# Performance work log

Hardware: AMD Instinct MI355X
Metric: run time of the kernel (lower is better)

The kernel has to match this reference:

```python
import jax, jax.numpy as jnp
import numpy as np

B, H, K, NUM_PTR, MAX_LEN = 32768, 896, 2000, 2, 128


def setup_inputs() -> dict:
    key = jax.random.key(0)
    k1, k2, k3 = jax.random.split(key, 3)
    z = jax.random.normal(k1, (B, H), dtype=jnp.float32)
    # codebook init: normal(0, 0.02) as in torch.nn.init.normal_
    emb = 0.02 * jax.random.normal(k2, (K, H), dtype=jnp.float32)
    # pointer heads: two Linear(H, MAX_LEN) layers, stacked
    W = jax.random.normal(k3, (NUM_PTR, MAX_LEN, H), dtype=jnp.float32) / np.float32(np.sqrt(H))
    b = jnp.zeros((NUM_PTR, MAX_LEN), dtype=jnp.float32)
    return {"z": z, "emb": emb, "W": W, "b": b, "prompt_len": 96}


def reference(z, emb, W, b, prompt_len):
    # --- quantize: L2 cdist + argmin + gather + straight-through ---
    # dist[b,k] = ||z_b||^2 - 2 z_b . e_k + ||e_k||^2   -> [B, K]
    dist = (jnp.sum(z * z, axis=1, keepdims=True)
            - 2.0 * (z @ emb.T)
            + jnp.sum(emb * emb, axis=1)[None, :])
    idx = jnp.argmin(dist, axis=1)            # [B]
    z_q = emb[idx]                            # [B, H]
    op_state = z + jax.lax.stop_gradient(z_q - z)
    # --- pointer heads with prompt-length mask ---
    logits = jnp.einsum('bh,plh->bpl', z, W) + b[None, :, :]   # [B, 2, MAX_LEN]
    mask = jnp.where(jnp.arange(logits.shape[-1]) < prompt_len, 0.0, -jnp.inf)
    ptr_logits = logits + mask[None, None, :]
    return op_state, ptr_logits
```

## Files before the change

### kernel.cpp

```cpp
#include <hip/hip_runtime.h>
#include <hip/hip_bf16.h>
#include <cstdint>
#include <cstddef>

#define B_SZ 32768
#define H_SZ 896
#define K_SZ 2000
#define KPAD 2048
#define NPTR_COLS 256
#define NCAT 2304
#define BM 128
#define BN 128
#define BK 32

typedef float floatx4 __attribute__((ext_vector_type(4)));
typedef __bf16 bf16x8 __attribute__((ext_vector_type(8)));

#define MASK_NEG 1.0e30f

__device__ inline unsigned short f2bf_rne(float x) {
  unsigned u = __builtin_bit_cast(unsigned, x);
  unsigned r = u + 0x7fffu + ((u >> 16) & 1u);
  return (unsigned short)(r >> 16);
}
__device__ inline float bf2f(unsigned short b) {
  unsigned u = ((unsigned)b) << 16;
  return __builtin_bit_cast(float, u);
}

typedef __attribute__((address_space(1))) void GV;
typedef __attribute__((address_space(3))) void LV;
__device__ inline void load_lds16(const void* gsrc, void* ldst) {
  __builtin_amdgcn_global_load_lds((GV*)gsrc, (LV*)ldst, 16, 0, 0);
}

__global__ __launch_bounds__(256) void convert_kernel(
    const float* __restrict__ emb, const float* __restrict__ W,
    unsigned short* __restrict__ cat_hi, unsigned short* __restrict__ cat_lo,
    float* __restrict__ normE) {
  const int row = blockIdx.x;
  const int tid = threadIdx.x;
  const float* src = nullptr;
  bool zero = false;
  if (row < K_SZ)       src = emb + (size_t)row * H_SZ;
  else if (row < KPAD)  zero = true;
  else                  src = W + (size_t)(row - KPAD) * H_SZ;

  float ss = 0.f;
  for (int c = tid; c < H_SZ; c += 256) {
    float x = zero ? 0.f : src[c];
    unsigned short hb = f2bf_rne(x);
    float hf = bf2f(hb);
    unsigned short lb = f2bf_rne(x - hf);
    cat_hi[(size_t)row * H_SZ + c] = hb;
    cat_lo[(size_t)row * H_SZ + c] = lb;
    ss += x * x;
  }
  #pragma unroll
  for (int off = 32; off > 0; off >>= 1) ss += __shfl_down(ss, off);
  __shared__ float wsum[4];
  const int wave = tid >> 6, lane = tid & 63;
  if (lane == 0) wsum[wave] = ss;
  __syncthreads();
  if (tid == 0 && row < KPAD) normE[row] = wsum[0] + wsum[1] + wsum[2] + wsum[3];
}

__global__ __launch_bounds__(256, 2) void main_gemm(
    const float* __restrict__ z,
    const unsigned short* __restrict__ cat_hi,
    const unsigned short* __restrict__ cat_lo,
    const float* __restrict__ normE,
    const float* __restrict__ bias,
    const int* __restrict__ plen_p,
    float* __restrict__ pmin, int* __restrict__ pidx,
    float* __restrict__ out_logits) {
  __shared__ unsigned short Ahi[BM * BK], Alo[BM * BK];
  __shared__ unsigned short Bhi[BN * BK], Blo[BN * BK];
  __shared__ float red_v[2][BM];
  __shared__ int   red_i[2][BM];

  const int tid = threadIdx.x;
  const int wave = tid >> 6, lane = tid & 63;
  const int wm = wave >> 1, wn = wave & 1;
  const int bx = blockIdx.x, split = blockIdx.y;
  const int b0 = bx * BM;
  const int lrow = lane & 15, lk = lane >> 4;

  float minv[16];
  int   mini[16];
  #pragma unroll
  for (int s = 0; s < 16; ++s) { minv[s] = 3.4e38f; mini[s] = 0; }

  const int t0 = split * 8;
  const int tcount = (split == 2) ? 2 : 8;

  const int arow = tid >> 1, ahalf = tid & 1;
  const float* zsrc = z + (size_t)(b0 + arow) * H_SZ + ahalf * 16;
  unsigned short* a_hi_dst = &Ahi[arow * BK + ahalf * 16];
  unsigned short* a_lo_dst = &Alo[arow * BK + ahalf * 16];

  for (int tt = t0; tt < t0 + tcount; ++tt) {
    const int n0 = tt * BN;
    floatx4 acc[4][4];
    #pragma unroll
    for (int i = 0; i < 4; ++i)
      #pragma unroll
      for (int j = 0; j < 4; ++j) acc[i][j] = (floatx4){0.f, 0.f, 0.f, 0.f};

    for (int kk = 0; kk < H_SZ; kk += BK) {
      float xv[16];
      #pragma unroll
      for (int q = 0; q < 4; ++q) {
        const float4 f = *(const float4*)(zsrc + kk + q * 4);
        xv[q * 4 + 0] = f.x; xv[q * 4 + 1] = f.y;
        xv[q * 4 + 2] = f.z; xv[q * 4 + 3] = f.w;
      }
      unsigned hv[8], lv[8];
      #pragma unroll
      for (int q = 0; q < 8; ++q) {
        unsigned short h0 = f2bf_rne(xv[2 * q]), h1 = f2bf_rne(xv[2 * q + 1]);
        float r0 = xv[2 * q] - bf2f(h0), r1 = xv[2 * q + 1] - bf2f(h1);
        unsigned short l0 = f2bf_rne(r0), l1 = f2bf_rne(r1);
        hv[q] = (unsigned)h0 | ((unsigned)h1 << 16);
        lv[q] = (unsigned)l0 | ((unsigned)l1 << 16);
      }
      *(uint4*)(a_hi_dst)     = make_uint4(hv[0], hv[1], hv[2], hv[3]);
      *(uint4*)(a_hi_dst + 8) = make_uint4(hv[4], hv[5], hv[6], hv[7]);
      *(uint4*)(a_lo_dst)     = make_uint4(lv[0], lv[1], lv[2], lv[3]);
      *(uint4*)(a_lo_dst + 8) = make_uint4(lv[4], lv[5], lv[6], lv[7]);

      #pragma unroll
      for (int s = 0; s < 2; ++s) {
        const int seg = wave * 2 + s;
        const int nrow = n0 + seg * 16 + (lane >> 2);
        const size_t goff = (size_t)nrow * H_SZ + kk + (lane & 3) * 8;
        load_lds16(cat_hi + goff, &Bhi[seg * 16 * BK]);
        load_lds16(cat_lo + goff, &Blo[seg * 16 * BK]);
      }
      __syncthreads();

      bf16x8 ah[4], al[4], bh[4], bl[4];
      #pragma unroll
      for (int i = 0; i < 4; ++i) {
        const int r = (wm * 64 + i * 16 + lrow) * BK + lk * 8;
        ah[i] = *(const bf16x8*)&Ahi[r];
        al[i] = *(const bf16x8*)&Alo[r];
      }
      #pragma unroll
      for (int j = 0; j < 4; ++j) {
        const int r = (wn * 64 + j * 16 + lrow) * BK + lk * 8;
        bh[j] = *(const bf16x8*)&Bhi[r];
        bl[j] = *(const bf16x8*)&Blo[r];
      }
      #pragma unroll
      for (int i = 0; i < 4; ++i)
        #pragma unroll
        for (int j = 0; j < 4; ++j) {
          acc[i][j] = __builtin_amdgcn_mfma_f32_16x16x32_bf16(ah[i], bh[j], acc[i][j], 0, 0, 0);
          acc[i][j] = __builtin_amdgcn_mfma_f32_16x16x32_bf16(ah[i], bl[j], acc[i][j], 0, 0, 0);
          acc[i][j] = __builtin_amdgcn_mfma_f32_16x16x32_bf16(al[i], bh[j], acc[i][j], 0, 0, 0);
        }
      __syncthreads();
    }

    if (split < 2) {
      #pragma unroll
      for (int j = 0; j < 4; ++j) {
        const int k = n0 + wn * 64 + j * 16 + lrow;
        const float nE = normE[k];
        const bool valid = (k < K_SZ);
        #pragma unroll
        for (int i = 0; i < 4; ++i)
          #pragma unroll
          for (int r = 0; r < 4; ++r) {
            float v = nE - 2.0f * acc[i][j][r];
            if (!valid) v = 3.4e38f;
            const int s = i * 4 + r;
            if (v < minv[s]) { minv[s] = v; mini[s] = k; }
          }
      }
    } else {
      const int plen = *plen_p;
      #pragma unroll
      for (int j = 0; j < 4; ++j) {
        const int c = (n0 - KPAD) + wn * 64 + j * 16 + lrow;
        const float bv = bias[c];
        const bool masked = ((c & 127) >= plen);
        #pragma unroll
        for (int i = 0; i < 4; ++i) {
          const int growbase = b0 + wm * 64 + i * 16 + lk * 4;
          #pragma unroll
          for (int r = 0; r < 4; ++r) {
            const float val = masked ? -MASK_NEG : (acc[i][j][r] + bv);
            out_logits[(size_t)(growbase + r) * NPTR_COLS + c] = val;
          }
        }
      }
    }
  }

  if (split < 2) {
    #pragma unroll
    for (int s = 0; s < 16; ++s) {
      float v = minv[s]; int id = mini[s];
      #pragma unroll
      for (int m = 1; m < 16; m <<= 1) {
        const float ov = __shfl_xor(v, m);
        const int   oid = __shfl_xor(id, m);
        if (ov < v || (ov == v && oid < id)) { v = ov; id = oid; }
      }
      if (lrow == 0) {
        const int row_local = wm * 64 + (s >> 2) * 16 + lk * 4 + (s & 3);
        red_v[wn][row_local] = v;
        red_i[wn][row_local] = id;
      }
    }
    __syncthreads();
    if (tid < BM) {
      const float v0 = red_v[0][tid], v1 = red_v[1][tid];
      float v; int id;
      if (v1 < v0) { v = v1; id = red_i[1][tid]; }
      else         { v = v0; id = red_i[0][tid]; }
      pmin[(size_t)split * B_SZ + b0 + tid] = v;
      pidx[(size_t)split * B_SZ + b0 + tid] = id;
    }
  }
}

__global__ __launch_bounds__(256) void merge_gather(
    const float* __restrict__ z, const float* __restrict__ emb,
    const float* __restrict__ pmin, const int* __restrict__ pidx,
    float* __restrict__ out0) {
  const int row = blockIdx.x;
  const float v0 = pmin[row], v1 = pmin[B_SZ + row];
  const int id = (v1 < v0) ? pidx[B_SZ + row] : pidx[row];
  const float4* e4 = (const float4*)(emb + (size_t)id * H_SZ);
  const float4* z4 = (const float4*)(z + (size_t)row * H_SZ);
  float4* o4 = (float4*)(out0 + (size_t)row * H_SZ);
  const int t = threadIdx.x;
  if (t < H_SZ / 4) {
    const float4 zz = z4[t], ee = e4[t];
    float4 r;
    r.x = zz.x + (ee.x - zz.x);
    r.y = zz.y + (ee.y - zz.y);
    r.z = zz.z + (ee.z - zz.z);
    r.w = zz.w + (ee.w - zz.w);
    o4[t] = r;
  }
}

extern "C" void kernel_launch(void* const* d_in, const int* in_sizes, int n_in,
                              void* d_out, int out_size, void* d_ws, size_t ws_size,
                              hipStream_t stream) {
  const float* z    = (const float*)d_in[0];
  const float* emb  = (const float*)d_in[1];
  const float* W    = (const float*)d_in[2];
  const float* bias = (const float*)d_in[3];
  const int*   plen = (const int*)d_in[4];
  float* out = (float*)d_out;

  char* ws = (char*)d_ws;
  unsigned short* cat_hi = (unsigned short*)(ws);
  unsigned short* cat_lo = (unsigned short*)(ws + 4128768);
  float* normE = (float*)(ws + 8257536);
  float* pmin  = (float*)(ws + 8265728);
  int*   pidx  = (int*)(ws + 8527872);
  float* out_logits = out + (size_t)B_SZ * H_SZ;

  convert_kernel<<<dim3(NCAT), dim3(256), 0, stream>>>(emb, W, cat_hi, cat_lo, normE);
  main_gemm<<<dim3(B_SZ / BM, 3), dim3(256), 0, stream>>>(
      z, cat_hi, cat_lo, normE, bias, plen, pmin, pidx, out_logits);
  merge_gather<<<dim3(B_SZ), dim3(256), 0, stream>>>(z, emb, pmin, pidx, out);
}
```

Measured before the change: 714.2 us.

## Pre-split z to bf16 hi/lo, swizzle LDS tiles, batch gather rows

Adds a convert_z pass that splits z into bf16 hi/lo planes once, so the GEMM loads A tiles straight into LDS with global_load_lds instead of re-converting fp32 z in every tile iteration across all splits. LDS layout is XOR-swizzled per 16-row segment to cut bank conflicts on the MFMA fragment reads, and launch bounds rise to 3 blocks per CU. merge_gather now handles 8 rows per block. The extra pass costs writing and re-reading about 117 MB of bf16 workspace, and it falls back to in-loop conversion when the workspace is too small.

Result: no change. 721.1 us (+1.0%).

```diff
diff --git a/kernel.cpp b/kernel.cpp
--- a/kernel.cpp
+++ b/kernel.cpp
@@ -13,6 +13,7 @@
 #define BN 128
 #define BK 32
 
+typedef unsigned short ushort_t;
 typedef float floatx4 __attribute__((ext_vector_type(4)));
 typedef __bf16 bf16x8 __attribute__((ext_vector_type(8)));
 
@@ -34,9 +35,9 @@
   __builtin_amdgcn_global_load_lds((GV*)gsrc, (LV*)ldst, 16, 0, 0);
 }
 
-__global__ __launch_bounds__(256) void convert_kernel(
+__global__ __launch_bounds__(256) void convert_cat(
     const float* __restrict__ emb, const float* __restrict__ W,
-    unsigned short* __restrict__ cat_hi, unsigned short* __restrict__ cat_lo,
+    ushort_t* __restrict__ cat_hi, ushort_t* __restrict__ cat_lo,
     float* __restrict__ normE) {
   const int row = blockIdx.x;
   const int tid = threadIdx.x;
@@ -65,17 +66,34 @@
   if (tid == 0 && row < KPAD) normE[row] = wsum[0] + wsum[1] + wsum[2] + wsum[3];
 }
 
-__global__ __launch_bounds__(256, 2) void main_gemm(
+__global__ __launch_bounds__(256) void convert_z(
+    const float* __restrict__ z, ushort_t* __restrict__ zhi,
+    ushort_t* __restrict__ zlo) {
+  const size_t g = (size_t)blockIdx.x * 256 + threadIdx.x;
+  const float4 f = ((const float4*)z)[g];
+  float xs[4] = {f.x, f.y, f.z, f.w};
+  ushort_t h[4], l[4];
+  #pragma unroll
+  for (int q = 0; q < 4; ++q) {
+    h[q] = f2bf_rne(xs[q]);
+    l[q] = f2bf_rne(xs[q] - bf2f(h[q]));
+  }
+  ((ushort4*)zhi)[g] = make_ushort4(h[0], h[1], h[2], h[3]);
+  ((ushort4*)zlo)[g] = make_ushort4(l[0], l[1], l[2], l[3]);
+}
+
+template <int PRESPLIT>
+__global__ __launch_bounds__(256, 3) void main_gemm(
     const float* __restrict__ z,
-    const unsigned short* __restrict__ cat_hi,
-    const unsigned short* __restrict__ cat_lo,
+    const ushort_t* __restrict__ zhi, const ushort_t* __restrict__ zlo,
+    const ushort_t* __restrict__ cat_hi, const ushort_t* __restrict__ cat_lo,
     const float* __restrict__ normE,
     const float* __restrict__ bias,
     const int* __restrict__ plen_p,
     float* __restrict__ pmin, int* __restrict__ pidx,
     float* __restrict__ out_logits) {
-  __shared__ unsigned short Ahi[BM * BK], Alo[BM * BK];
-  __shared__ unsigned short Bhi[BN * BK], Blo[BN * BK];
+  __shared__ ushort_t Ahi[BM * BK], Alo[BM * BK];
+  __shared__ ushort_t Bhi[BN * BK], Blo[BN * BK];
   __shared__ float red_v[2][BM];
   __shared__ int   red_i[2][BM];
 
@@ -86,6 +104,10 @@
   const int b0 = bx * BM;
   const int lrow = lane & 15, lk = lane >> 4;
 
+  const int srow = lane >> 2;
+  const int schunk = (lane & 3) ^ ((lane >> 3) & 3);
+  const int aswz = (lrow >> 1) & 3;
+
   float minv[16];
   int   mini[16];
   #pragma unroll
@@ -96,8 +118,10 @@
 
   const int arow = tid >> 1, ahalf = tid & 1;
   const float* zsrc = z + (size_t)(b0 + arow) * H_SZ + ahalf * 16;
-  unsigned short* a_hi_dst = &Ahi[arow * BK + ahalf * 16];
-  unsigned short* a_lo_dst = &Alo[arow * BK + ahalf * 16];
+  const int abase = (arow >> 4) * 512 + (arow & 15) * 32;
+  const int awz = (arow >> 1) & 3;
+  const int ac0 = ((ahalf * 2) ^ awz) << 3;
+  const int ac1 = ((ahalf * 2 + 1) ^ awz) << 3;
 
   for (int tt = t0; tt < t0 + tcount; ++tt) {
     const int n0 = tt * BN;
@@ -108,49 +132,55 @@
       for (int j = 0; j < 4; ++j) acc[i][j] = (floatx4){0.f, 0.f, 0.f, 0.f};
 
     for (int kk = 0; kk < H_SZ; kk += BK) {
-      float xv[16];
-      #pragma unroll
-      for (int q = 0; q < 4; ++q) {
-        const float4 f = *(const float4*)(zsrc + kk + q * 4);
-        xv[q * 4 + 0] = f.x; xv[q * 4 + 1] = f.y;
-        xv[q * 4 + 2] = f.z; xv[q * 4 + 3] = f.w;
-      }
-      unsigned hv[8], lv[8];
-      #pragma unroll
-      for (int q = 0; q < 8; ++q) {
-        unsigned short h0 = f2bf_rne(xv[2 * q]), h1 = f2bf_rne(xv[2 * q + 1]);
-        float r0 = xv[2 * q] - bf2f(h0), r1 = xv[2 * q + 1] - bf2f(h1);
-        unsigned short l0 = f2bf_rne(r0), l1 = f2bf_rne(r1);
-        hv[q] = (unsigned)h0 | ((unsigned)h1 << 16);
-        lv[q] = (unsigned)l0 | ((unsigned)l1 << 16);
-      }
-      *(uint4*)(a_hi_dst)     = make_uint4(hv[0], hv[1], hv[2], hv[3]);
-      *(uint4*)(a_hi_dst + 8) = make_uint4(hv[4], hv[5], hv[6], hv[7]);
-      *(uint4*)(a_lo_dst)     = make_uint4(lv[0], lv[1], lv[2], lv[3]);
-      *(uint4*)(a_lo_dst + 8) = make_uint4(lv[4], lv[5], lv[6], lv[7]);
-
       #pragma unroll
       for (int s = 0; s < 2; ++s) {
         const int seg = wave * 2 + s;
-        const int nrow = n0 + seg * 16 + (lane >> 2);
-        const size_t goff = (size_t)nrow * H_SZ + kk + (lane & 3) * 8;
-        load_lds16(cat_hi + goff, &Bhi[seg * 16 * BK]);
-        load_lds16(cat_lo + goff, &Blo[seg * 16 * BK]);
+        const int r = seg * 16 + srow;
+        const size_t bo = (size_t)(n0 + r) * H_SZ + kk + schunk * 8;
+        load_lds16(cat_hi + bo, &Bhi[seg * 512]);
+        load_lds16(cat_lo + bo, &Blo[seg * 512]);
+        if (PRESPLIT) {
+          const size_t ao = (size_t)(b0 + r) * H_SZ + kk + schunk * 8;
+          load_lds16(zhi + ao, &Ahi[seg * 512]);
+          load_lds16(zlo + ao, &Alo[seg * 512]);
+        }
+      }
+      if (!PRESPLIT) {
+        float xv[16];
+        #pragma unroll
+        for (int q = 0; q < 4; ++q) {
+          const float4 f = *(const float4*)(zsrc + kk + q * 4);
+          xv[q * 4 + 0] = f.x; xv[q * 4 + 1] = f.y;
+          xv[q * 4 + 2] = f.z; xv[q * 4 + 3] = f.w;
+        }
+        unsigned hv[8], lv[8];
+        #pragma unroll
+        for (int q = 0; q < 8; ++q) {
+          unsigned short h0 = f2bf_rne(xv[2 * q]), h1 = f2bf_rne(xv[2 * q + 1]);
+          float r0 = xv[2 * q] - bf2f(h0), r1 = xv[2 * q + 1] - bf2f(h1);
+          unsigned short l0 = f2bf_rne(r0), l1 = f2bf_rne(r1);
+          hv[q] = (unsigned)h0 | ((unsigned)h1 << 16);
+          lv[q] = (unsigned)l0 | ((unsigned)l1 << 16);
+        }
+        *(uint4*)&Ahi[abase + ac0] = make_uint4(hv[0], hv[1], hv[2], hv[3]);
+        *(uint4*)&Ahi[abase + ac1] = make_uint4(hv[4], hv[5], hv[6], hv[7]);
+        *(uint4*)&Alo[abase + ac0] = make_uint4(lv[0], lv[1], lv[2], lv[3]);
+        *(uint4*)&Alo[abase + ac1] = make_uint4(lv[4], lv[5], lv[6], lv[7]);
       }
       __syncthreads();
 
       bf16x8 ah[4], al[4], bh[4], bl[4];
       #pragma unroll
       for (int i = 0; i < 4; ++i) {
-        const int r = (wm * 64 + i * 16 + lrow) * BK + lk * 8;
-        ah[i] = *(const bf16x8*)&Ahi[r];
-        al[i] = *(const bf16x8*)&Alo[r];
+        const int off = (wm * 4 + i) * 512 + lrow * 32 + ((lk ^ aswz) << 3);
+        ah[i] = *(const bf16x8*)&Ahi[off];
+        al[i] = *(const bf16x8*)&Alo[off];
       }
       #pragma unroll
       for (int j = 0; j < 4; ++j) {
-        const int r = (wn * 64 + j * 16 + lrow) * BK + lk * 8;
-        bh[j] = *(const bf16x8*)&Bhi[r];
-        bl[j] = *(const bf16x8*)&Blo[r];
+        const int off = (wn * 4 + j) * 512 + lrow * 32 + ((lk ^ aswz) << 3);
+        bh[j] = *(const bf16x8*)&Bhi[off];
+        bl[j] = *(const bf16x8*)&Blo[off];
       }
       #pragma unroll
       for (int i = 0; i < 4; ++i)
@@ -231,21 +261,21 @@
     const float* __restrict__ z, const float* __restrict__ emb,
     const float* __restrict__ pmin, const int* __restrict__ pidx,
     float* __restrict__ out0) {
-  const int row = blockIdx.x;
-  const float v0 = pmin[row], v1 = pmin[B_SZ + row];
-  const int id = (v1 < v0) ? pidx[B_SZ + row] : pidx[row];
-  const float4* e4 = (const float4*)(emb + (size_t)id * H_SZ);
-  const float4* z4 = (const float4*)(z + (size_t)row * H_SZ);
-  float4* o4 = (float4*)(out0 + (size_t)row * H_SZ);
-  const int t = threadIdx.x;
-  if (t < H_SZ / 4) {
-    const float4 zz = z4[t], ee = e4[t];
+  const int base_row = blockIdx.x * 8;
+  for (int u = threadIdx.x; u < 8 * 224; u += 256) {
+    const int lr = u / 224;
+    const int c = u - lr * 224;
+    const int row = base_row + lr;
+    const float v0 = pmin[row], v1 = pmin[B_SZ + row];
+    const int id = (v1 < v0) ? pidx[B_SZ + row] : pidx[row];
+    const float4 zz = ((const float4*)(z + (size_t)row * H_SZ))[c];
+    const float4 ee = ((const float4*)(emb + (size_t)id * H_SZ))[c];
     float4 r;
     r.x = zz.x + (ee.x - zz.x);
     r.y = zz.y + (ee.y - zz.y);
     r.z = zz.z + (ee.z - zz.z);
     r.w = zz.w + (ee.w - zz.w);
-    o4[t] = r;
+    ((float4*)(out0 + (size_t)row * H_SZ))[c] = r;
   }
 }
 
@@ -260,15 +290,27 @@
   float* out = (float*)d_out;
 
   char* ws = (char*)d_ws;
-  unsigned short* cat_hi = (unsigned short*)(ws);
-  unsigned short* cat_lo = (unsigned short*)(ws + 4128768);
-  float* normE = (float*)(ws + 8257536);
-  float* pmin  = (float*)(ws + 8265728);
-  int*   pidx  = (int*)(ws + 8527872);
+  const size_t CAT_BYTES = (size_t)NCAT * H_SZ * 2;
+  const size_t Z_BYTES   = (size_t)B_SZ * H_SZ * 2;
+  ushort_t* cat_hi = (ushort_t*)(ws);
+  ushort_t* cat_lo = (ushort_t*)(ws + CAT_BYTES);
+  float* normE = (float*)(ws + 2 * CAT_BYTES);
+  float* pmin  = (float*)(ws + 2 * CAT_BYTES + 16384);
+  int*   pidx  = (int*)(ws + 2 * CAT_BYTES + 16384 + 262144);
+  ushort_t* zhi = (ushort_t*)(ws + 2 * CAT_BYTES + 16384 + 2 * 262144);
+  ushort_t* zlo = (ushort_t*)((char*)zhi + Z_BYTES);
+  const size_t REQ = 2 * CAT_BYTES + 16384 + 2 * 262144 + 2 * Z_BYTES;
+
   float* out_logits = out + (size_t)B_SZ * H_SZ;
 
-  convert_kernel<<<dim3(NCAT), dim3(256), 0, stream>>>(emb, W, cat_hi, cat_lo, normE);
-  main_gemm<<<dim3(B_SZ / BM, 3), dim3(256), 0, stream>>>(
-      z, cat_hi, cat_lo, normE, bias, plen, pmin, pidx, out_logits);
-  merge_gather<<<dim3(B_SZ), dim3(256), 0, stream>>>(z, emb, pmin, pidx, out);
-}
+  convert_cat<<<dim3(NCAT), dim3(256), 0, stream>>>(emb, W, cat_hi, cat_lo, normE);
+  if (ws_size >= REQ) {
+    convert_z<<<dim3(B_SZ * H_SZ / 1024), dim3(256), 0, stream>>>(z, zhi, zlo);
+    main_gemm<1><<<dim3(B_SZ / BM, 3), dim3(256), 0, stream>>>(
+        z, zhi, zlo, cat_hi, cat_lo, normE, bias, plen, pmin, pidx, out_logits);
+  } else {
+    main_gemm<0><<<dim3(B_SZ / BM, 3), dim3(256), 0, stream>>>(
+        z, zhi, zlo, cat_hi, cat_lo, normE, bias, plen, pmin, pidx, out_logits);
+  }
+  merge_gather<<<dim3(B_SZ / 8), dim3(256), 0, stream>>>(z, emb, pmin, pidx, out);
+}
```
